# Kernel optimization log

Hardware: AMD Instinct MI355X
Metric: run time of the kernel (lower is better)

The kernel has to match this reference:

```python
import jax, jax.numpy as jnp
import numpy as np

EPS = 1e-12

def l2_normalize(x, axis=-1):
    # matches torch F.normalize(p=2, dim=1, eps=1e-12) for 2D input
    n = jnp.sqrt(jnp.sum(x * x, axis=axis, keepdims=True))
    return x / jnp.maximum(n, EPS)

def setup_inputs() -> dict:
    key = jax.random.key(0)
    ks = jax.random.split(key, 7)
    N, D = 8192, 256
    s = 1.0 / np.sqrt(D)
    x = jax.random.normal(ks[0], (N, D), dtype=jnp.float32)
    Wq = jax.random.uniform(ks[1], (D, D), jnp.float32, -s, s)
    bq = jax.random.uniform(ks[2], (D,), jnp.float32, -s, s)
    Wk = jax.random.uniform(ks[3], (D, D), jnp.float32, -s, s)
    bk = jax.random.uniform(ks[4], (D,), jnp.float32, -s, s)
    Wv = jax.random.uniform(ks[5], (D, D), jnp.float32, -s, s)
    bv = jax.random.uniform(ks[6], (D,), jnp.float32, -s, s)
    return {"x": x, "Wq": Wq, "bq": bq, "Wk": Wk, "bk": bk, "Wv": Wv, "bv": bv}

def reference(x, Wq, bq, Wk, bk, Wv, bv):
    q = l2_normalize(x @ Wq.T + bq)           # [N, D]
    k = l2_normalize(x @ Wk.T + bk)           # [N, D]
    v = x @ Wv.T + bv                         # [N, D]
    cos_sim = q @ k.T                         # [N, N]
    w = jax.nn.relu(cos_sim)
    # zero diagonal, then renormalize rows to sum 1
    N = w.shape[0]
    w = jnp.where(jnp.eye(N, dtype=bool), 0.0, w)
    w = w / jnp.maximum(jnp.sum(w, axis=-1, keepdims=True), EPS)
    return w @ v + x
```

## Files before the change

kernel.cpp:

```cpp
#include <hip/hip_runtime.h>

#define NROWS 8192
#define DDIM  256
#define KSPLIT 4
#define BM 128
#define BK 64
#define NT (NROWS / KSPLIT / BK)

typedef __bf16 bf16x8 __attribute__((ext_vector_type(8)));
typedef float  f32x4  __attribute__((ext_vector_type(4)));
typedef float  f32x16 __attribute__((ext_vector_type(16)));

typedef __attribute__((address_space(1))) unsigned int uint_gas;
typedef __attribute__((address_space(3))) unsigned int uint_las;

__device__ __forceinline__ void gload_lds16(const void* g, void* l) {
  __builtin_amdgcn_global_load_lds((const uint_gas*)g, (uint_las*)l, 16, 0, 0);
}

__device__ __forceinline__ unsigned int f2bf_bits(float f) {
  union { float f; unsigned int u; } v; v.f = f;
  unsigned int r = v.u + 0x7FFFu + ((v.u >> 16) & 1u);
  return r >> 16;
}
__device__ __forceinline__ float bf2f(unsigned int b) {
  union { unsigned int u; float f; } v; v.u = b << 16;
  return v.f;
}
__device__ __forceinline__ unsigned int pack2bf(float a, float b) {
  union { unsigned int u; __bf16 h[2]; } p;
  p.h[0] = (__bf16)a; p.h[1] = (__bf16)b;
  return p.u;
}

__global__ __launch_bounds__(256) void convert_kernel(
    const float* __restrict__ wq, const float* __restrict__ wk,
    const float* __restrict__ wv, unsigned short* __restrict__ Wb)
{
  int i = blockIdx.x * 256 + threadIdx.x;
  const int nw4 = DDIM * DDIM / 4;
  const float4* src; int j;
  if (i < nw4)          { src = (const float4*)wq; j = i; }
  else if (i < 2*nw4)   { src = (const float4*)wk; j = i - nw4; }
  else                  { src = (const float4*)wv; j = i - 2*nw4; }
  float4 f = src[j];
  ushort4 o;
  o.x = (unsigned short)f2bf_bits(f.x);
  o.y = (unsigned short)f2bf_bits(f.y);
  o.z = (unsigned short)f2bf_bits(f.z);
  o.w = (unsigned short)f2bf_bits(f.w);
  ((ushort4*)(Wb))[i] = o;
}

__global__ __launch_bounds__(256) void qkv_kernel(
    const float* __restrict__ bq, const float* __restrict__ bk, const float* __restrict__ bv,
    const float* __restrict__ x, const unsigned short* __restrict__ Wb,
    unsigned short* __restrict__ qb, unsigned short* __restrict__ kb,
    unsigned short* __restrict__ vb, unsigned short* __restrict__ vT)
{
  __shared__ unsigned short vstage[DDIM * 72];
  const int t = threadIdx.x;
  const int w = t >> 6, l = t & 63;
  const int c = l & 15, g = l >> 4;
  const int out = blockIdx.x / 128;
  const int mb  = blockIdx.x % 128;
  const int row0 = mb * 64;
  const int rw = row0 + w * 16;

  bf16x8 a[8];
  #pragma unroll
  for (int ks = 0; ks < 8; ks++) {
    const float* p = x + (size_t)(rw + c) * DDIM + ks * 32 + g * 8;
    float4 f0 = *(const float4*)p;
    float4 f1 = *(const float4*)(p + 4);
    union { bf16x8 v; unsigned short s[8]; } u;
    u.s[0] = (unsigned short)f2bf_bits(f0.x);
    u.s[1] = (unsigned short)f2bf_bits(f0.y);
    u.s[2] = (unsigned short)f2bf_bits(f0.z);
    u.s[3] = (unsigned short)f2bf_bits(f0.w);
    u.s[4] = (unsigned short)f2bf_bits(f1.x);
    u.s[5] = (unsigned short)f2bf_bits(f1.y);
    u.s[6] = (unsigned short)f2bf_bits(f1.z);
    u.s[7] = (unsigned short)f2bf_bits(f1.w);
    a[ks] = u.v;
  }

  const unsigned short* W = Wb + out * DDIM * DDIM;
  const float* bias = (out == 0) ? bq : (out == 1) ? bk : bv;
  unsigned short* dst = (out == 0) ? qb : (out == 1) ? kb : vb;
  f32x4 vals[16];
  #pragma unroll
  for (int ct = 0; ct < 16; ct++) {
    f32x4 acc = {0.f, 0.f, 0.f, 0.f};
    #pragma unroll
    for (int ks = 0; ks < 8; ks++) {
      bf16x8 b = *(const bf16x8*)(W + (size_t)(ct * 16 + c) * DDIM + ks * 32 + g * 8);
      acc = __builtin_amdgcn_mfma_f32_16x16x32_bf16(a[ks], b, acc, 0, 0, 0);
    }
    float bias_v = bias[ct * 16 + c];
    #pragma unroll
    for (int r = 0; r < 4; r++) acc[r] += bias_v;
    vals[ct] = acc;
  }
  if (out < 2) {
    #pragma unroll
    for (int r = 0; r < 4; r++) {
      float ss = 0.f;
      #pragma unroll
      for (int ct = 0; ct < 16; ct++) ss += vals[ct][r] * vals[ct][r];
      ss += __shfl_xor(ss, 1); ss += __shfl_xor(ss, 2);
      ss += __shfl_xor(ss, 4); ss += __shfl_xor(ss, 8);
      float inv = 1.f / fmaxf(sqrtf(ss), 1e-12f);
      #pragma unroll
      for (int ct = 0; ct < 16; ct++) vals[ct][r] *= inv;
    }
  }
  #pragma unroll
  for (int ct = 0; ct < 16; ct++) {
    #pragma unroll
    for (int r = 0; r < 4; r++) {
      unsigned int bits = f2bf_bits(vals[ct][r]);
      unsigned int ob = (unsigned int)__shfl_xor((int)bits, 1);
      if (!(l & 1))
        *(unsigned int*)(dst + (size_t)(rw + g * 4 + r) * DDIM + ct * 16 + c) =
            bits | (ob << 16);
      if (out == 2)
        vstage[(ct * 16 + c) * 72 + (w * 16 + g * 4 + r)] = (unsigned short)bits;
    }
  }
  if (out == 2) {
    __syncthreads();
    #pragma unroll
    for (int p = 0; p < 8; p++) {
      int dd = (t >> 3) + p * 32;
      int ch = t & 7;
      *(uint4*)(vT + (size_t)dd * NROWS + row0 + ch * 8) =
          *(const uint4*)(vstage + dd * 72 + ch * 8);
    }
  }
}

__global__ __launch_bounds__(512, 2) void attn_kernel(
    const unsigned short* __restrict__ qb, const unsigned short* __restrict__ kb,
    const unsigned short* __restrict__ vT,
    float* __restrict__ nump, float* __restrict__ denp)
{
  __shared__ __align__(16) char smem[147456];
  char* kbuf = smem;
  char* vbuf = smem + 65536;
  char* P    = smem + 131072;

  const int t = threadIdx.x;
  const int w = t >> 6, l = t & 63;
  const int l31 = l & 31, hi = l >> 5;
  const int sr = w >> 1, sc = w & 1;
  const int pr = w >> 2, pc = w & 3;
  const int bid = blockIdx.x;
  const int split = bid & (KSPLIT - 1);
  const int mb = bid >> 2;
  const int q0 = mb * BM;
  const int kbase0 = split * (NROWS / KSPLIT);

  const char* kbc = (const char*)kb;
  const char* vtc = (const char*)vT;

  bf16x8 qa[16];
  {
    const unsigned short* qrowp = qb + (size_t)(q0 + sr * 32 + l31) * DDIM + hi * 8;
    #pragma unroll
    for (int m = 0; m < 16; m++)
      qa[m] = *(const bf16x8*)(qrowp + m * 16);
  }

  f32x16 oacc[2][2];
  #pragma unroll
  for (int rt = 0; rt < 2; rt++)
    #pragma unroll
    for (int dt = 0; dt < 2; dt++)
      oacc[rt][dt] = (f32x16){0.f};
  float denl = 0.f;

  auto stage = [&](int buf, int it) {
    const int kbase = kbase0 + it * BK;
    const char* ksrc = kbc + (size_t)kbase * 512;
    #pragma unroll
    for (int i = 0; i < 4; i++) {
      int n = i * 512 + t;
      int row = n >> 5, slot = n & 31;
      gload_lds16(ksrc + row * 512 + ((slot ^ (row & 7)) * 16),
                  kbuf + buf * 32768 + i * 8192 + w * 1024);
    }
    const char* vsrc = vtc + (size_t)kbase * 2;
    #pragma unroll
    for (int i = 0; i < 4; i++) {
      int n = i * 512 + t;
      int dd = n >> 3, slot = n & 7;
      gload_lds16(vsrc + (size_t)dd * (NROWS * 2) + ((slot ^ (dd & 7)) * 16),
                  vbuf + buf * 32768 + i * 8192 + w * 1024);
    }
  };

  stage(0, 0);
  asm volatile("s_waitcnt vmcnt(0)" ::: "memory");
  __builtin_amdgcn_sched_barrier(0);
  __builtin_amdgcn_s_barrier();
  __builtin_amdgcn_sched_barrier(0);

  for (int it = 0; it < NT; ++it) {
    const int cur = it & 1;
    if (it + 1 < NT) stage(cur ^ 1, it + 1);
    __builtin_amdgcn_sched_barrier(0);

    const char* kcur = kbuf + cur * 32768;
    const int krl = sc * 32 + l31;
    f32x16 sacc = {0.f};
    #pragma unroll
    for (int m = 0; m < 16; m++) {
      bf16x8 kf = *(const bf16x8*)(kcur + krl * 512 + ((m * 32 + hi * 16) ^ ((krl & 7) << 4)));
      sacc = __builtin_amdgcn_mfma_f32_32x32x16_bf16(kf, qa[m], sacc, 0, 0, 0);
    }
    {
      const int qrow = sr * 32 + l31;
      char* prow = P + qrow * 128;
      const int swz = (qrow & 7) << 4;
      #pragma unroll
      for (int j = 0; j < 4; j++) {
        float v0 = fmaxf(sacc[4 * j + 0], 0.f);
        float v1 = fmaxf(sacc[4 * j + 1], 0.f);
        float v2 = fmaxf(sacc[4 * j + 2], 0.f);
        float v3 = fmaxf(sacc[4 * j + 3], 0.f);
        denl += (v0 + v1) + (v2 + v3);
        uint2 d2;
        d2.x = pack2bf(v0, v1);
        d2.y = pack2bf(v2, v3);
        *(uint2*)(prow + ((sc * 64 + j * 16 + hi * 8) ^ swz)) = d2;
      }
    }
    asm volatile("s_waitcnt lgkmcnt(0)" ::: "memory");
    __builtin_amdgcn_sched_barrier(0);
    __builtin_amdgcn_s_barrier();
    __builtin_amdgcn_sched_barrier(0);

    const char* vcur = vbuf + cur * 32768;
    #pragma unroll
    for (int ch = 0; ch < 4; ch++) {
      bf16x8 pa[2], vf[2];
      #pragma unroll
      for (int rt = 0; rt < 2; rt++) {
        int qrow = pr * 64 + rt * 32 + l31;
        pa[rt] = *(const bf16x8*)(P + qrow * 128 +
                                  ((ch * 32 + hi * 16) ^ ((qrow & 7) << 4)));
      }
      #pragma unroll
      for (int dt = 0; dt < 2; dt++) {
        int dl = pc * 64 + dt * 32 + l31;
        vf[dt] = *(const bf16x8*)(vcur + dl * 128 +
                                  ((ch * 32 + hi * 16) ^ ((dl & 7) << 4)));
      }
      #pragma unroll
      for (int rt = 0; rt < 2; rt++)
        #pragma unroll
        for (int dt = 0; dt < 2; dt++)
          oacc[rt][dt] = __builtin_amdgcn_mfma_f32_32x32x16_bf16(pa[rt], vf[dt],
                                                                 oacc[rt][dt], 0, 0, 0);
    }
    asm volatile("s_waitcnt vmcnt(0)" ::: "memory");
    __builtin_amdgcn_sched_barrier(0);
    __builtin_amdgcn_s_barrier();
    __builtin_amdgcn_sched_barrier(0);
  }

  float* np = nump + (size_t)split * NROWS * DDIM;
  #pragma unroll
  for (int rt = 0; rt < 2; rt++)
    #pragma unroll
    for (int dt = 0; dt < 2; dt++)
      #pragma unroll
      for (int r = 0; r < 16; r++) {
        int rowg = q0 + pr * 64 + rt * 32 + (r & 3) + 8 * (r >> 2) + 4 * hi;
        int col  = pc * 64 + dt * 32 + l31;
        np[(size_t)rowg * DDIM + col] = oacc[rt][dt][r];
      }
  {
    float d = denl;
    d += __shfl_xor(d, 32);
    if (l < 32)
      denp[((size_t)split * 2 + sc) * NROWS + q0 + sr * 32 + l] = d;
  }
}

__global__ __launch_bounds__(256) void combine_kernel(
    const float* __restrict__ x, const unsigned short* __restrict__ qb,
    const unsigned short* __restrict__ kb, const unsigned short* __restrict__ vb,
    const float* __restrict__ nump, const float* __restrict__ denp,
    float* __restrict__ out)
{
  const int t = threadIdx.x;
  const int w = t >> 6, l = t & 63;
  const int i = blockIdx.x * 4 + w;

  ushort4 q4 = *(const ushort4*)(qb + (size_t)i * DDIM + l * 4);
  ushort4 k4 = *(const ushort4*)(kb + (size_t)i * DDIM + l * 4);
  float s = bf2f(q4.x) * bf2f(k4.x) + bf2f(q4.y) * bf2f(k4.y)
          + bf2f(q4.z) * bf2f(k4.z) + bf2f(q4.w) * bf2f(k4.w);
  #pragma unroll
  for (int m = 1; m < 64; m <<= 1) s += __shfl_xor(s, m);
  float r  = fmaxf(s, 0.f);
  float rb = bf2f(f2bf_bits(r));

  float den = 0.f;
  #pragma unroll
  for (int sp = 0; sp < KSPLIT * 2; sp++)
    den += denp[(size_t)sp * NROWS + i];
  float inv = 1.f / fmaxf(den - rb, 1e-12f);

  const int d0 = l * 4;
  float4 acc = *(const float4*)(nump + (size_t)i * DDIM + d0);
  #pragma unroll
  for (int sp = 1; sp < KSPLIT; sp++) {
    float4 a2 = *(const float4*)(nump + (size_t)sp * NROWS * DDIM + (size_t)i * DDIM + d0);
    acc.x += a2.x; acc.y += a2.y; acc.z += a2.z; acc.w += a2.w;
  }
  ushort4 v4 = *(const ushort4*)(vb + (size_t)i * DDIM + d0);
  float4 xx = *(const float4*)(x + (size_t)i * DDIM + d0);
  float4 o;
  o.x = (acc.x - rb * bf2f(v4.x)) * inv + xx.x;
  o.y = (acc.y - rb * bf2f(v4.y)) * inv + xx.y;
  o.z = (acc.z - rb * bf2f(v4.z)) * inv + xx.z;
  o.w = (acc.w - rb * bf2f(v4.w)) * inv + xx.w;
  *(float4*)(out + (size_t)i * DDIM + d0) = o;
}

extern "C" void kernel_launch(void* const* d_in, const int* in_sizes, int n_in,
                              void* d_out, int out_size, void* d_ws, size_t ws_size,
                              hipStream_t stream)
{
  const float* x  = (const float*)d_in[0];
  const float* Wq = (const float*)d_in[1];
  const float* bq = (const float*)d_in[2];
  const float* Wk = (const float*)d_in[3];
  const float* bk = (const float*)d_in[4];
  const float* Wv = (const float*)d_in[5];
  const float* bv = (const float*)d_in[6];

  char* ws = (char*)d_ws;
  unsigned short* Wb  = (unsigned short*)(ws + 0);
  unsigned short* qb  = (unsigned short*)(ws + 393216);
  unsigned short* kb  = (unsigned short*)(ws + 4587520);
  unsigned short* vb  = (unsigned short*)(ws + 8781824);
  unsigned short* vT  = (unsigned short*)(ws + 12976128);
  float* nump = (float*)(ws + 17170432);
  float* denp = (float*)(ws + 50724864);

  convert_kernel<<<192, 256, 0, stream>>>(Wq, Wk, Wv, Wb);
  qkv_kernel<<<384, 256, 0, stream>>>(bq, bk, bv, x, Wb, qb, kb, vb, vT);
  attn_kernel<<<(NROWS / BM) * KSPLIT, 512, 0, stream>>>(qb, kb, vT, nump, denp);
  combine_kernel<<<NROWS / 4, 256, 0, stream>>>(x, qb, kb, vb, nump, denp, (float*)d_out);
}
```

Baseline: 132.1 us.

## Enlarge attention tile, fp16 partials, and fuse weight conversion into QKV

The attention kernel now uses 256-row query tiles with each wave owning 32 query rows, computing two 32-key score tiles and a 64x128 output slab per wave. The key split rises from 4 to 8 and occupancy drops to one block per CU. Partial numerators are stored as fp16 instead of fp32 to cut the write and read traffic of the split reduction. The separate weight-conversion kernel is removed, and the QKV kernel converts fp32 weights inline, which trades a launch for redundant conversion work and some fp16 precision risk.

```diff
diff --git a/kernel.cpp b/kernel.cpp
--- a/kernel.cpp
+++ b/kernel.cpp
@@ -2,8 +2,8 @@
 
 #define NROWS 8192
 #define DDIM  256
-#define KSPLIT 4
-#define BM 128
+#define KSPLIT 8
+#define BM 256
 #define BK 64
 #define NT (NROWS / KSPLIT / BK)
 
@@ -32,29 +32,33 @@
   p.h[0] = (__bf16)a; p.h[1] = (__bf16)b;
   return p.u;
 }
-
-__global__ __launch_bounds__(256) void convert_kernel(
-    const float* __restrict__ wq, const float* __restrict__ wk,
-    const float* __restrict__ wv, unsigned short* __restrict__ Wb)
-{
-  int i = blockIdx.x * 256 + threadIdx.x;
-  const int nw4 = DDIM * DDIM / 4;
-  const float4* src; int j;
-  if (i < nw4)          { src = (const float4*)wq; j = i; }
-  else if (i < 2*nw4)   { src = (const float4*)wk; j = i - nw4; }
-  else                  { src = (const float4*)wv; j = i - 2*nw4; }
-  float4 f = src[j];
-  ushort4 o;
-  o.x = (unsigned short)f2bf_bits(f.x);
-  o.y = (unsigned short)f2bf_bits(f.y);
-  o.z = (unsigned short)f2bf_bits(f.z);
-  o.w = (unsigned short)f2bf_bits(f.w);
-  ((ushort4*)(Wb))[i] = o;
+__device__ __forceinline__ unsigned short f2h_bits(float f) {
+  union { _Float16 h; unsigned short u; } c; c.h = (_Float16)f;
+  return c.u;
+}
+__device__ __forceinline__ float h2f(unsigned short u) {
+  union { unsigned short u; _Float16 h; } c; c.u = u;
+  return (float)c.h;
+}
+__device__ __forceinline__ bf16x8 cvt8(const float* p) {
+  float4 f0 = *(const float4*)p;
+  float4 f1 = *(const float4*)(p + 4);
+  union { bf16x8 v; unsigned short s[8]; } u;
+  u.s[0] = (unsigned short)f2bf_bits(f0.x);
+  u.s[1] = (unsigned short)f2bf_bits(f0.y);
+  u.s[2] = (unsigned short)f2bf_bits(f0.z);
+  u.s[3] = (unsigned short)f2bf_bits(f0.w);
+  u.s[4] = (unsigned short)f2bf_bits(f1.x);
+  u.s[5] = (unsigned short)f2bf_bits(f1.y);
+  u.s[6] = (unsigned short)f2bf_bits(f1.z);
+  u.s[7] = (unsigned short)f2bf_bits(f1.w);
+  return u.v;
 }
 
 __global__ __launch_bounds__(256) void qkv_kernel(
     const float* __restrict__ bq, const float* __restrict__ bk, const float* __restrict__ bv,
-    const float* __restrict__ x, const unsigned short* __restrict__ Wb,
+    const float* __restrict__ x,
+    const float* __restrict__ wq, const float* __restrict__ wk, const float* __restrict__ wv,
     unsigned short* __restrict__ qb, unsigned short* __restrict__ kb,
     unsigned short* __restrict__ vb, unsigned short* __restrict__ vT)
 {
@@ -69,23 +73,10 @@
 
   bf16x8 a[8];
   #pragma unroll
-  for (int ks = 0; ks < 8; ks++) {
-    const float* p = x + (size_t)(rw + c) * DDIM + ks * 32 + g * 8;
-    float4 f0 = *(const float4*)p;
-    float4 f1 = *(const float4*)(p + 4);
-    union { bf16x8 v; unsigned short s[8]; } u;
-    u.s[0] = (unsigned short)f2bf_bits(f0.x);
-    u.s[1] = (unsigned short)f2bf_bits(f0.y);
-    u.s[2] = (unsigned short)f2bf_bits(f0.z);
-    u.s[3] = (unsigned short)f2bf_bits(f0.w);
-    u.s[4] = (unsigned short)f2bf_bits(f1.x);
-    u.s[5] = (unsigned short)f2bf_bits(f1.y);
-    u.s[6] = (unsigned short)f2bf_bits(f1.z);
-    u.s[7] = (unsigned short)f2bf_bits(f1.w);
-    a[ks] = u.v;
-  }
-
-  const unsigned short* W = Wb + out * DDIM * DDIM;
+  for (int ks = 0; ks < 8; ks++)
+    a[ks] = cvt8(x + (size_t)(rw + c) * DDIM + ks * 32 + g * 8);
+
+  const float* Wf = (out == 0) ? wq : (out == 1) ? wk : wv;
   const float* bias = (out == 0) ? bq : (out == 1) ? bk : bv;
   unsigned short* dst = (out == 0) ? qb : (out == 1) ? kb : vb;
   f32x4 vals[16];
@@ -94,7 +85,7 @@
     f32x4 acc = {0.f, 0.f, 0.f, 0.f};
     #pragma unroll
     for (int ks = 0; ks < 8; ks++) {
-      bf16x8 b = *(const bf16x8*)(W + (size_t)(ct * 16 + c) * DDIM + ks * 32 + g * 8);
+      bf16x8 b = cvt8(Wf + (size_t)(ct * 16 + c) * DDIM + ks * 32 + g * 8);
       acc = __builtin_amdgcn_mfma_f32_16x16x32_bf16(a[ks], b, acc, 0, 0, 0);
     }
     float bias_v = bias[ct * 16 + c];
@@ -140,12 +131,12 @@
   }
 }
 
-__global__ __launch_bounds__(512, 2) void attn_kernel(
+__global__ __launch_bounds__(512, 1) void attn_kernel(
     const unsigned short* __restrict__ qb, const unsigned short* __restrict__ kb,
     const unsigned short* __restrict__ vT,
-    float* __restrict__ nump, float* __restrict__ denp)
+    unsigned short* __restrict__ nump, float* __restrict__ denp)
 {
-  __shared__ __align__(16) char smem[147456];
+  __shared__ __align__(16) char smem[163840];
   char* kbuf = smem;
   char* vbuf = smem + 65536;
   char* P    = smem + 131072;
@@ -153,11 +144,10 @@
   const int t = threadIdx.x;
   const int w = t >> 6, l = t & 63;
   const int l31 = l & 31, hi = l >> 5;
-  const int sr = w >> 1, sc = w & 1;
-  const int pr = w >> 2, pc = w & 3;
+  const int a = w >> 1, h = w & 1;
   const int bid = blockIdx.x;
   const int split = bid & (KSPLIT - 1);
-  const int mb = bid >> 2;
+  const int mb = bid >> 3;
   const int q0 = mb * BM;
   const int kbase0 = split * (NROWS / KSPLIT);
 
@@ -166,18 +156,18 @@
 
   bf16x8 qa[16];
   {
-    const unsigned short* qrowp = qb + (size_t)(q0 + sr * 32 + l31) * DDIM + hi * 8;
+    const unsigned short* qrowp = qb + (size_t)(q0 + w * 32 + l31) * DDIM + hi * 8;
     #pragma unroll
     for (int m = 0; m < 16; m++)
       qa[m] = *(const bf16x8*)(qrowp + m * 16);
   }
 
-  f32x16 oacc[2][2];
-  #pragma unroll
-  for (int rt = 0; rt < 2; rt++)
-    #pragma unroll
-    for (int dt = 0; dt < 2; dt++)
-      oacc[rt][dt] = (f32x16){0.f};
+  f32x16 oacc[2][4];
+  #pragma unroll
+  for (int tt = 0; tt < 2; tt++)
+    #pragma unroll
+    for (int dt = 0; dt < 4; dt++)
+      oacc[tt][dt] = (f32x16){0.f};
   float denl = 0.f;
 
   auto stage = [&](int buf, int it) {
@@ -212,28 +202,30 @@
     __builtin_amdgcn_sched_barrier(0);
 
     const char* kcur = kbuf + cur * 32768;
-    const int krl = sc * 32 + l31;
-    f32x16 sacc = {0.f};
-    #pragma unroll
-    for (int m = 0; m < 16; m++) {
-      bf16x8 kf = *(const bf16x8*)(kcur + krl * 512 + ((m * 32 + hi * 16) ^ ((krl & 7) << 4)));
-      sacc = __builtin_amdgcn_mfma_f32_32x32x16_bf16(kf, qa[m], sacc, 0, 0, 0);
-    }
-    {
-      const int qrow = sr * 32 + l31;
-      char* prow = P + qrow * 128;
-      const int swz = (qrow & 7) << 4;
-      #pragma unroll
-      for (int j = 0; j < 4; j++) {
-        float v0 = fmaxf(sacc[4 * j + 0], 0.f);
-        float v1 = fmaxf(sacc[4 * j + 1], 0.f);
-        float v2 = fmaxf(sacc[4 * j + 2], 0.f);
-        float v3 = fmaxf(sacc[4 * j + 3], 0.f);
+    const int qrow = w * 32 + l31;
+    char* prow = P + qrow * 128;
+    const int pswz = (qrow & 7) << 4;
+    #pragma unroll
+    for (int c = 0; c < 2; c++) {
+      const int krl = c * 32 + l31;
+      const int kswz = (krl & 7) << 4;
+      f32x16 sacc = (f32x16){0.f};
+      #pragma unroll
+      for (int m = 0; m < 16; m++) {
+        bf16x8 kf = *(const bf16x8*)(kcur + krl * 512 + ((m * 32 + hi * 16) ^ kswz));
+        sacc = __builtin_amdgcn_mfma_f32_32x32x16_bf16(kf, qa[m], sacc, 0, 0, 0);
+      }
+      #pragma unroll
+      for (int q = 0; q < 4; q++) {
+        float v0 = fmaxf(sacc[4 * q + 0], 0.f);
+        float v1 = fmaxf(sacc[4 * q + 1], 0.f);
+        float v2 = fmaxf(sacc[4 * q + 2], 0.f);
+        float v3 = fmaxf(sacc[4 * q + 3], 0.f);
         denl += (v0 + v1) + (v2 + v3);
         uint2 d2;
         d2.x = pack2bf(v0, v1);
         d2.y = pack2bf(v2, v3);
-        *(uint2*)(prow + ((sc * 64 + j * 16 + hi * 8) ^ swz)) = d2;
+        *(uint2*)(prow + ((c * 64 + q * 16 + hi * 8) ^ pswz)) = d2;
       }
     }
     asm volatile("s_waitcnt lgkmcnt(0)" ::: "memory");
@@ -242,27 +234,20 @@
     __builtin_amdgcn_sched_barrier(0);
 
     const char* vcur = vbuf + cur * 32768;
+    const int pr0 = a * 64 + l31;
+    const int pr1 = a * 64 + 32 + l31;
     #pragma unroll
     for (int ch = 0; ch < 4; ch++) {
-      bf16x8 pa[2], vf[2];
-      #pragma unroll
-      for (int rt = 0; rt < 2; rt++) {
-        int qrow = pr * 64 + rt * 32 + l31;
-        pa[rt] = *(const bf16x8*)(P + qrow * 128 +
-                                  ((ch * 32 + hi * 16) ^ ((qrow & 7) << 4)));
+      const int cb = ch * 32 + hi * 16;
+      bf16x8 pa0 = *(const bf16x8*)(P + pr0 * 128 + (cb ^ ((pr0 & 7) << 4)));
+      bf16x8 pa1 = *(const bf16x8*)(P + pr1 * 128 + (cb ^ ((pr1 & 7) << 4)));
+      #pragma unroll
+      for (int dt = 0; dt < 4; dt++) {
+        int dl = h * 128 + dt * 32 + l31;
+        bf16x8 vf = *(const bf16x8*)(vcur + dl * 128 + (cb ^ ((dl & 7) << 4)));
+        oacc[0][dt] = __builtin_amdgcn_mfma_f32_32x32x16_bf16(pa0, vf, oacc[0][dt], 0, 0, 0);
+        oacc[1][dt] = __builtin_amdgcn_mfma_f32_32x32x16_bf16(pa1, vf, oacc[1][dt], 0, 0, 0);
       }
-      #pragma unroll
-      for (int dt = 0; dt < 2; dt++) {
-        int dl = pc * 64 + dt * 32 + l31;
-        vf[dt] = *(const bf16x8*)(vcur + dl * 128 +
-                                  ((ch * 32 + hi * 16) ^ ((dl & 7) << 4)));
-      }
-      #pragma unroll
-      for (int rt = 0; rt < 2; rt++)
-        #pragma unroll
-        for (int dt = 0; dt < 2; dt++)
-          oacc[rt][dt] = __builtin_amdgcn_mfma_f32_32x32x16_bf16(pa[rt], vf[dt],
-                                                                 oacc[rt][dt], 0, 0, 0);
     }
     asm volatile("s_waitcnt vmcnt(0)" ::: "memory");
     __builtin_amdgcn_sched_barrier(0);
@@ -270,29 +255,29 @@
     __builtin_amdgcn_sched_barrier(0);
   }
 
-  float* np = nump + (size_t)split * NROWS * DDIM;
-  #pragma unroll
-  for (int rt = 0; rt < 2; rt++)
-    #pragma unroll
-    for (int dt = 0; dt < 2; dt++)
+  unsigned short* np = nump + (size_t)split * NROWS * DDIM;
+  #pragma unroll
+  for (int tt = 0; tt < 2; tt++)
+    #pragma unroll
+    for (int dt = 0; dt < 4; dt++)
       #pragma unroll
       for (int r = 0; r < 16; r++) {
-        int rowg = q0 + pr * 64 + rt * 32 + (r & 3) + 8 * (r >> 2) + 4 * hi;
-        int col  = pc * 64 + dt * 32 + l31;
-        np[(size_t)rowg * DDIM + col] = oacc[rt][dt][r];
+        int rowg = q0 + a * 64 + tt * 32 + (r & 3) + 8 * (r >> 2) + 4 * hi;
+        int col  = h * 128 + dt * 32 + l31;
+        np[(size_t)rowg * DDIM + col] = f2h_bits(oacc[tt][dt][r]);
       }
   {
     float d = denl;
     d += __shfl_xor(d, 32);
     if (l < 32)
-      denp[((size_t)split * 2 + sc) * NROWS + q0 + sr * 32 + l] = d;
+      denp[(size_t)split * NROWS + q0 + w * 32 + l] = d;
   }
 }
 
 __global__ __launch_bounds__(256) void combine_kernel(
     const float* __restrict__ x, const unsigned short* __restrict__ qb,
     const unsigned short* __restrict__ kb, const unsigned short* __restrict__ vb,
-    const float* __restrict__ nump, const float* __restrict__ denp,
+    const unsigned short* __restrict__ nump, const float* __restrict__ denp,
     float* __restrict__ out)
 {
   const int t = threadIdx.x;
@@ -310,16 +295,17 @@
 
   float den = 0.f;
   #pragma unroll
-  for (int sp = 0; sp < KSPLIT * 2; sp++)
+  for (int sp = 0; sp < KSPLIT; sp++)
     den += denp[(size_t)sp * NROWS + i];
   float inv = 1.f / fmaxf(den - rb, 1e-12f);
 
   const int d0 = l * 4;
-  float4 acc = *(const float4*)(nump + (size_t)i * DDIM + d0);
-  #pragma unroll
-  for (int sp = 1; sp < KSPLIT; sp++) {
-    float4 a2 = *(const float4*)(nump + (size_t)sp * NROWS * DDIM + (size_t)i * DDIM + d0);
-    acc.x += a2.x; acc.y += a2.y; acc.z += a2.z; acc.w += a2.w;
+  float4 acc = {0.f, 0.f, 0.f, 0.f};
+  #pragma unroll
+  for (int sp = 0; sp < KSPLIT; sp++) {
+    ushort4 u4 = *(const ushort4*)(nump + ((size_t)sp * NROWS + i) * DDIM + d0);
+    acc.x += h2f(u4.x); acc.y += h2f(u4.y);
+    acc.z += h2f(u4.z); acc.w += h2f(u4.w);
   }
   ushort4 v4 = *(const ushort4*)(vb + (size_t)i * DDIM + d0);
   float4 xx = *(const float4*)(x + (size_t)i * DDIM + d0);
@@ -344,16 +330,14 @@
   const float* bv = (const float*)d_in[6];
 
   char* ws = (char*)d_ws;
-  unsigned short* Wb  = (unsigned short*)(ws + 0);
-  unsigned short* qb  = (unsigned short*)(ws + 393216);
-  unsigned short* kb  = (unsigned short*)(ws + 4587520);
-  unsigned short* vb  = (unsigned short*)(ws + 8781824);
-  unsigned short* vT  = (unsigned short*)(ws + 12976128);
-  float* nump = (float*)(ws + 17170432);
-  float* denp = (float*)(ws + 50724864);
-
-  convert_kernel<<<192, 256, 0, stream>>>(Wq, Wk, Wv, Wb);
-  qkv_kernel<<<384, 256, 0, stream>>>(bq, bk, bv, x, Wb, qb, kb, vb, vT);
+  unsigned short* qb  = (unsigned short*)(ws + 0);
+  unsigned short* kb  = (unsigned short*)(ws + 4194304);
+  unsigned short* vb  = (unsigned short*)(ws + 8388608);
+  unsigned short* vT  = (unsigned short*)(ws + 12582912);
+  unsigned short* nump = (unsigned short*)(ws + 16777216);
+  float* denp = (float*)(ws + 50331648);
+
+  qkv_kernel<<<384, 256, 0, stream>>>(bq, bk, bv, x, Wq, Wk, Wv, qb, kb, vb, vT);
   attn_kernel<<<(NROWS / BM) * KSPLIT, 512, 0, stream>>>(qb, kb, vT, nump, denp);
   combine_kernel<<<NROWS / 4, 256, 0, stream>>>(x, qb, kb, vb, nump, denp, (float*)d_out);
 }
```

Measured after the change: 183.8 us. 39.2% more time.
